# Optimization experiments

Measured on AMD Instinct MI355X. Metric: run time of the kernel, lower is better.

The kernel has to match this reference:

```python
import jax, jax.numpy as jnp
import numpy as np

QD, KD, HID, NH = 256, 320, 256, 8
NQ, NK, NB = 4096, 4096, 16
DH = HID // NH
EPS = 1e-5
SCALE = float(1.0 / np.sqrt(DH))


def setup_inputs() -> dict:
    key = jax.random.key(0)
    ks = jax.random.split(key, 12)
    s = 0.02
    return {
        "query_nodes": jax.random.normal(ks[0], (NQ, QD), jnp.float32),
        "key_nodes": jax.random.normal(ks[1], (NK, KD), jnp.float32),
        "Wq": jax.random.normal(ks[2], (QD, HID), jnp.float32) * s,
        "bq": jnp.zeros((HID,), jnp.float32),
        "Wk": jax.random.normal(ks[3], (KD, HID), jnp.float32) * s,
        "bk": jnp.zeros((HID,), jnp.float32),
        "Wv": jax.random.normal(ks[4], (KD, HID), jnp.float32) * s,
        "bv": jnp.zeros((HID,), jnp.float32),
        "in_proj_w": jax.random.normal(ks[5], (3 * HID, HID), jnp.float32) * s,
        "in_proj_b": jnp.zeros((3 * HID,), jnp.float32),
        "mha_ow": jax.random.normal(ks[6], (HID, HID), jnp.float32) * s,
        "mha_ob": jnp.zeros((HID,), jnp.float32),
        "Wo": jax.random.normal(ks[7], (HID, QD), jnp.float32) * s,
        "bo": jnp.zeros((QD,), jnp.float32),
        "ln_g": jnp.ones((QD,), jnp.float32),
        "ln_b": jnp.zeros((QD,), jnp.float32),
        "query_batch_idx": jnp.sort(jax.random.randint(ks[8], (NQ,), 0, NB, jnp.int32)),
        "key_batch_idx": jnp.sort(jax.random.randint(ks[9], (NK,), 0, NB, jnp.int32)),
    }


def reference(query_nodes, key_nodes, Wq, bq, Wk, bk, Wv, bv, in_proj_w, in_proj_b,
              mha_ow, mha_ob, Wo, bo, ln_g, ln_b, query_batch_idx, key_batch_idx):
    # outer projections
    q = query_nodes @ Wq + bq          # [NQ, HID]
    k = key_nodes @ Wk + bk            # [NK, HID]
    v = key_nodes @ Wv + bv            # [NK, HID]
    # nn.MultiheadAttention internal in_proj (weights stored [3H, H], applied as x @ W.T)
    q2 = q @ in_proj_w[:HID].T + in_proj_b[:HID]
    k2 = k @ in_proj_w[HID:2 * HID].T + in_proj_b[HID:2 * HID]
    v2 = v @ in_proj_w[2 * HID:].T + in_proj_b[2 * HID:]
    qh = q2.reshape(NQ, NH, DH)
    kh = k2.reshape(NK, NH, DH)
    vh = v2.reshape(NK, NH, DH)
    scores = jnp.einsum('qhd,khd->hqk', qh, kh) * SCALE   # [NH, NQ, NK]
    mask = query_batch_idx[:, None] != key_batch_idx[None, :]  # True = disallowed
    scores = jnp.where(mask[None], -jnp.inf, scores)
    attn = jax.nn.softmax(scores, axis=-1)
    ctx = jnp.einsum('hqk,khd->qhd', attn, vh).reshape(NQ, HID)
    ctx = ctx @ mha_ow + mha_ob        # MHA internal out_proj
    out = ctx @ Wo + bo                # module out_proj back to query_dim
    x = query_nodes + out              # residual (dropout is identity in eval)
    mu = jnp.mean(x, axis=-1, keepdims=True)
    var = jnp.mean((x - mu) ** 2, axis=-1, keepdims=True)
    return (x - mu) / jnp.sqrt(var + EPS) * ln_g + ln_b
```

## Files before the change

kernel.cpp:

```cpp
#include <hip/hip_runtime.h>
#include <hip/hip_bf16.h>
#include <math.h>

#define NQ 4096
#define NK 4096
#define QD 256
#define KD 320
#define HID 256
#define NH 8
#define DH 32
#define NB 16
#define LN_EPS 1e-5f
#define ATT_SCALE 0.17677669529663687f

typedef unsigned short ushort_t;
typedef __attribute__((ext_vector_type(8))) short bf16x8_t;
typedef __attribute__((ext_vector_type(4))) short bf16x4_t;
typedef __attribute__((ext_vector_type(4))) float f32x4_t;

#define OFF_Q2B   0
#define OFF_K2B   524288
#define OFF_V2B   1048576
#define OFF_CTXB  1572864
#define OFF_WQT   2097152
#define OFF_WKT   2129920
#define OFF_WVT   2170880
#define OFF_WOT   2211840
#define OFF_BEFF  2244608
#define OFF_KST   2245632
#define OFF_KEN   2245648
#define OFF_FLAG  2245664

struct KArgs {
    const void* in[18];
    float* ws;
    void* out;
};

__device__ __forceinline__ float bf16_bits_to_f(ushort_t s) {
    unsigned int u = (unsigned int)s << 16;
    float f;
    __builtin_memcpy(&f, &u, 4);
    return f;
}

__device__ __forceinline__ ushort_t f_to_bf16_bits(float v) {
    __hip_bfloat16 t = (__hip_bfloat16)v;
    ushort_t b;
    __builtin_memcpy(&b, &t, 2);
    return b;
}

template <bool F32>
__device__ __forceinline__ bf16x8_t ld8(const void* p, size_t idx) {
    if constexpr (!F32) {
        return *(const bf16x8_t*)((const ushort_t*)p + idx);
    } else {
        f32x4_t f0 = *(const f32x4_t*)((const float*)p + idx);
        f32x4_t f1 = *(const f32x4_t*)((const float*)p + idx + 4);
        bf16x8_t h;
#pragma unroll
        for (int e = 0; e < 4; ++e) h[e] = (short)f_to_bf16_bits(f0[e]);
#pragma unroll
        for (int e = 0; e < 4; ++e) h[4 + e] = (short)f_to_bf16_bits(f1[e]);
        return h;
    }
}

template <bool F32>
__device__ __forceinline__ float ld1f(const void* p, size_t idx) {
    if constexpr (F32) return ((const float*)p)[idx];
    else               return bf16_bits_to_f(((const ushort_t*)p)[idx]);
}

template <bool F32>
__device__ __forceinline__ ushort_t ld1h(const void* p, size_t idx) {
    if constexpr (F32) return f_to_bf16_bits(((const float*)p)[idx]);
    else               return ((const ushort_t*)p)[idx];
}

__device__ __forceinline__ int detect_flag(const void* probe_v, int tid) {
    __shared__ float s_red[4];
    const ushort_t* probe = (const ushort_t*)probe_v;
    float mx = 0.f;
    for (int i = tid; i < 4096; i += 256) {
        float f = fabsf(bf16_bits_to_f(probe[i]));
        if (!(f == f)) f = 1e38f;
        mx = fmaxf(mx, f);
    }
    for (int off = 32; off; off >>= 1) mx = fmaxf(mx, __shfl_xor(mx, off, 64));
    if ((tid & 63) == 0) s_red[tid >> 6] = mx;
    __syncthreads();
    float m2 = fmaxf(fmaxf(s_red[0], s_red[1]), fmaxf(s_red[2], s_red[3]));
    __syncthreads();
    return (m2 < 100.f) ? 1 : 0;
}

template <bool F32>
__device__ __forceinline__ void fuse_qkv_tile(const void* A, size_t abase,
                                              const void* B, ushort_t* Out,
                                              int N, int m0, int n0,
                                              int col, int quad) {
    f32x4_t acc[4];
#pragma unroll
    for (int t = 0; t < 4; ++t) acc[t] = (f32x4_t){0.f, 0.f, 0.f, 0.f};
    size_t aoff = abase + (size_t)(m0 + col) * 256 + quad * 8;
    size_t boff = (size_t)(n0 + col) * 256 + quad * 8;
#pragma unroll
    for (int kc = 0; kc < 256; kc += 32) {
        bf16x8_t af = ld8<F32>(A, aoff + kc);
#pragma unroll
        for (int t = 0; t < 4; ++t) {
            bf16x8_t bf = ld8<F32>(B, boff + (size_t)t * 16 * 256 + kc);
            acc[t] = __builtin_amdgcn_mfma_f32_16x16x32_bf16(af, bf, acc[t], 0, 0, 0);
        }
    }
#pragma unroll
    for (int t = 0; t < 4; ++t)
#pragma unroll
        for (int rr = 0; rr < 4; ++rr)
            Out[(size_t)(m0 + quad * 4 + rr) * N + n0 + t * 16 + col] =
                f_to_bf16_bits(acc[t][rr]);
}

template <bool F32>
__device__ __forceinline__ void fuse_o_tile(const void* Wo, const void* Mow,
                                            ushort_t* Out, int m0, int n0,
                                            int col, int quad) {
    f32x4_t acc[4];
#pragma unroll
    for (int t = 0; t < 4; ++t) acc[t] = (f32x4_t){0.f, 0.f, 0.f, 0.f};
#pragma unroll
    for (int kc = 0; kc < 256; kc += 32) {
        bf16x8_t af;
#pragma unroll
        for (int t = 0; t < 8; ++t)
            af[t] = (short)ld1h<F32>(Wo, (size_t)(kc + quad * 8 + t) * 256 + m0 + col);
#pragma unroll
        for (int t = 0; t < 4; ++t) {
            bf16x8_t bf = ld8<F32>(Mow, (size_t)(n0 + t * 16 + col) * 256 + quad * 8 + kc);
            acc[t] = __builtin_amdgcn_mfma_f32_16x16x32_bf16(af, bf, acc[t], 0, 0, 0);
        }
    }
#pragma unroll
    for (int t = 0; t < 4; ++t)
#pragma unroll
        for (int rr = 0; rr < 4; ++rr)
            Out[(size_t)(m0 + quad * 4 + rr) * 256 + n0 + t * 16 + col] =
                f_to_bf16_bits(acc[t][rr]);
}

template <bool F32>
__device__ __forceinline__ void bias_body(KArgs& a, float* ws, int m, int tid) {
    __shared__ float bsh[256];
    float* beff = ws + OFF_BEFF;
    if (m < 3) {
        const void* bsrc = (m == 0) ? a.in[3] : (m == 1) ? a.in[5] : a.in[7];
        bsh[tid] = ld1f<F32>(bsrc, tid);
        __syncthreads();
        float acc = 0.f;
        size_t row = (size_t)(m * 256 + tid) * 256;
#pragma unroll 4
        for (int kc = 0; kc < 256; kc += 8) {
            bf16x8_t wr = ld8<F32>(a.in[8], row + kc);
#pragma unroll
            for (int t = 0; t < 8; ++t)
                acc += bsh[kc + t] * bf16_bits_to_f((ushort_t)wr[t]);
        }
        acc += ld1f<F32>(a.in[9], m * 256 + tid);
        beff[m * 256 + tid] = acc;
    } else {
        bsh[tid] = ld1f<F32>(a.in[11], tid);
        __syncthreads();
        float acc = 0.f;
        for (int k = 0; k < 256; ++k)
            acc += bsh[k] * ld1f<F32>(a.in[12], (size_t)k * 256 + tid);
        acc += ld1f<F32>(a.in[13], tid);
        beff[3 * 256 + tid] = acc;
    }
}

__global__ __launch_bounds__(256) void k_fuse(KArgs a) {
    float* ws = a.ws;
    const int tid = threadIdx.x, bid = blockIdx.x;
    const int lane = tid & 63, wv = tid >> 6;
    const int col = lane & 15, quad = lane >> 4;
    int fl = detect_flag(a.in[0], tid);
    if (bid == 0 && tid == 0) *(int*)(ws + OFF_FLAG) = fl;

    if (bid < 16) {
        const int* kb = (const int*)a.in[17];
        int* kstart = (int*)(ws + OFF_KST);
        int* kend   = (int*)(ws + OFF_KEN);
        int j = bid * 256 + tid;
        if (j < NK) {
            int b = kb[j];
            if (j == 0) {
                for (int x = 0; x < b; ++x) { kstart[x] = 0; kend[x] = 0; }
                kstart[b] = 0;
            } else {
                int bp = kb[j - 1];
                if (bp != b) {
                    kend[bp] = j;
                    for (int x = bp + 1; x < b; ++x) { kstart[x] = j; kend[x] = j; }
                    kstart[b] = j;
                }
            }
            if (j == NK - 1) {
                kend[b] = NK;
                for (int x = b + 1; x < NB; ++x) { kstart[x] = NK; kend[x] = NK; }
            }
        }
    } else if (bid < 88) {
        int r = bid - 16;
        const void* A; const void* B; ushort_t* Out;
        size_t abase; int N, mb, nb, typ;
        if (r < 16)      { typ = 0; A = a.in[8]; abase = 0;      B = a.in[2]; Out = (ushort_t*)(ws + OFF_WQT); N = 256; mb = r >> 2; nb = r & 3; }
        else if (r < 36) { typ = 0; int rr = r - 16; A = a.in[8]; abase = 65536;  B = a.in[4]; Out = (ushort_t*)(ws + OFF_WKT); N = 320; mb = rr / 5; nb = rr % 5; }
        else if (r < 56) { typ = 0; int rr = r - 36; A = a.in[8]; abase = 131072; B = a.in[6]; Out = (ushort_t*)(ws + OFF_WVT); N = 320; mb = rr / 5; nb = rr % 5; }
        else             { typ = 1; int rr = r - 56; A = a.in[12]; abase = 0; B = a.in[10]; Out = (ushort_t*)(ws + OFF_WOT); N = 256; mb = rr >> 2; nb = rr & 3; }
        int m0 = mb * 64 + wv * 16, n0 = nb * 64;
        if (typ == 0) {
            if (fl) fuse_qkv_tile<false>(A, abase, B, Out, N, m0, n0, col, quad);
            else    fuse_qkv_tile<true >(A, abase, B, Out, N, m0, n0, col, quad);
        } else {
            if (fl) fuse_o_tile<false>(A, B, Out, m0, n0, col, quad);
            else    fuse_o_tile<true >(A, B, Out, m0, n0, col, quad);
        }
    } else {
        int m = bid - 88;
        if (fl) bias_body<false>(a, ws, m, tid);
        else    bias_body<true >(a, ws, m, tid);
    }
}

template <bool F32, int KK>
__device__ __forceinline__ void proj_body(const void* X, const ushort_t* WT,
                                          const float* bias, ushort_t* Z,
                                          int m0, int n0, int col, int quad) {
    f32x4_t acc[4];
#pragma unroll
    for (int t = 0; t < 4; ++t) acc[t] = (f32x4_t){0.f, 0.f, 0.f, 0.f};
    size_t aoff = (size_t)(m0 + col) * KK + quad * 8;
    const ushort_t* Wrow = WT + (size_t)(n0 + col) * KK + quad * 8;
#pragma unroll
    for (int kc = 0; kc < KK; kc += 32) {
        bf16x8_t af = ld8<F32>(X, aoff + kc);
#pragma unroll
        for (int t = 0; t < 4; ++t) {
            bf16x8_t bf = *(const bf16x8_t*)(Wrow + (size_t)t * 16 * KK + kc);
            acc[t] = __builtin_amdgcn_mfma_f32_16x16x32_bf16(af, bf, acc[t], 0, 0, 0);
        }
    }
#pragma unroll
    for (int t = 0; t < 4; ++t)
#pragma unroll
        for (int rr = 0; rr < 4; ++rr) {
            int n = n0 + t * 16 + col;
            Z[(size_t)(m0 + quad * 4 + rr) * 256 + n] =
                f_to_bf16_bits(acc[t][rr] + bias[n]);
        }
}

__global__ __launch_bounds__(256) void k_qkv(KArgs a) {
    float* ws = a.ws;
    const int tid = threadIdx.x, u = blockIdx.x;
    const int lane = tid & 63, wv = tid >> 6;
    const int col = lane & 15, quad = lane >> 4;
    const int fl = *(const int*)(ws + OFF_FLAG);
    const float* beff = ws + OFF_BEFF;

    if (u < 256) {
        int m0 = (u >> 2) * 64 + wv * 16, n0 = (u & 3) * 64;
        const ushort_t* WT = (const ushort_t*)(ws + OFF_WQT);
        ushort_t* Z = (ushort_t*)(ws + OFF_Q2B);
        if (fl) proj_body<false, 256>(a.in[0], WT, beff, Z, m0, n0, col, quad);
        else    proj_body<true , 256>(a.in[0], WT, beff, Z, m0, n0, col, quad);
    } else if (u < 512) {
        int uu = u - 256;
        int m0 = (uu >> 2) * 64 + wv * 16, n0 = (uu & 3) * 64;
        const ushort_t* WT = (const ushort_t*)(ws + OFF_WKT);
        ushort_t* Z = (ushort_t*)(ws + OFF_K2B);
        if (fl) proj_body<false, 320>(a.in[1], WT, beff + 256, Z, m0, n0, col, quad);
        else    proj_body<true , 320>(a.in[1], WT, beff + 256, Z, m0, n0, col, quad);
    } else {
        int uu = u - 512;
        int m0 = (uu >> 2) * 64 + wv * 16, n0 = (uu & 3) * 64;
        const ushort_t* WT = (const ushort_t*)(ws + OFF_WVT);
        ushort_t* Z = (ushort_t*)(ws + OFF_V2B);
        if (fl) proj_body<false, 320>(a.in[1], WT, beff + 512, Z, m0, n0, col, quad);
        else    proj_body<true , 320>(a.in[1], WT, beff + 512, Z, m0, n0, col, quad);
    }
}

#define CTXP 264

template <bool F32>
__device__ __forceinline__ void oln_part(KArgs& a, float* ws,
                                         const ushort_t ctxl[16][CTXP],
                                         float sred[8][16], float ssred[8][16],
                                         int q0, int wv, int col, int quad,
                                         int fl) {
    const ushort_t* wot  = (const ushort_t*)(ws + OFF_WOT);
    const float* beffO = ws + OFF_BEFF + 3 * 256;

    f32x4_t acc[2];
#pragma unroll
    for (int t = 0; t < 2; ++t) acc[t] = (f32x4_t){0.f, 0.f, 0.f, 0.f};
    const ushort_t* Wbase = wot + (size_t)col * 256 + quad * 8;
#pragma unroll
    for (int kc = 0; kc < 256; kc += 32) {
        bf16x8_t af = *(const bf16x8_t*)(&ctxl[col][quad * 8 + kc]);
#pragma unroll
        for (int tt = 0; tt < 2; ++tt) {
            int t = wv * 2 + tt;
            bf16x8_t bf = *(const bf16x8_t*)(Wbase + (size_t)t * 16 * 256 + kc);
            acc[tt] = __builtin_amdgcn_mfma_f32_16x16x32_bf16(af, bf, acc[tt], 0, 0, 0);
        }
    }
    float s_[4] = {0.f, 0.f, 0.f, 0.f};
    float ss_[4] = {0.f, 0.f, 0.f, 0.f};
#pragma unroll
    for (int tt = 0; tt < 2; ++tt) {
        int n = (wv * 2 + tt) * 16 + col;
        float b = beffO[n];
#pragma unroll
        for (int rr = 0; rr < 4; ++rr) {
            int m = q0 + quad * 4 + rr;
            float x = acc[tt][rr] + b + ld1f<F32>(a.in[0], (size_t)m * 256 + n);
            acc[tt][rr] = x;
            s_[rr] += x;
            ss_[rr] += x * x;
        }
    }
#pragma unroll
    for (int off = 1; off < 16; off <<= 1) {
#pragma unroll
        for (int rr = 0; rr < 4; ++rr) {
            s_[rr]  += __shfl_xor(s_[rr],  off, 16);
            ss_[rr] += __shfl_xor(ss_[rr], off, 16);
        }
    }
    if (col == 0) {
#pragma unroll
        for (int rr = 0; rr < 4; ++rr) {
            sred[wv][quad * 4 + rr]  = s_[rr];
            ssred[wv][quad * 4 + rr] = ss_[rr];
        }
    }
    __syncthreads();
    float mu[4], inv[4];
#pragma unroll
    for (int rr = 0; rr < 4; ++rr) {
        int row = quad * 4 + rr;
        float ts = 0.f, tss = 0.f;
#pragma unroll
        for (int w = 0; w < 8; ++w) { ts += sred[w][row]; tss += ssred[w][row]; }
        mu[rr] = ts * (1.f / QD);
        float var = tss * (1.f / QD) - mu[rr] * mu[rr];
        inv[rr] = rsqrtf(var + LN_EPS);
    }
#pragma unroll
    for (int tt = 0; tt < 2; ++tt) {
        int n = (wv * 2 + tt) * 16 + col;
        float g = ld1f<F32>(a.in[14], n), bb = ld1f<F32>(a.in[15], n);
#pragma unroll
        for (int rr = 0; rr < 4; ++rr) {
            int m = q0 + quad * 4 + rr;
            float y = (acc[tt][rr] - mu[rr]) * inv[rr] * g + bb;
            size_t idx = (size_t)m * 256 + n;
            if (fl) ((ushort_t*)a.out)[idx] = f_to_bf16_bits(y);
            else    ((float*)a.out)[idx] = y;
        }
    }
}

__global__ __launch_bounds__(512) void k_attn_oln(KArgs a) {
    __shared__ ushort_t ctxl[16][CTXP];
    __shared__ float sred[8][16], ssred[8][16];
    float* ws = a.ws;
    const ushort_t* q2b = (const ushort_t*)(ws + OFF_Q2B);
    const ushort_t* k2b = (const ushort_t*)(ws + OFF_K2B);
    const ushort_t* v2b = (const ushort_t*)(ws + OFF_V2B);
    const ushort_t* ctxb = (const ushort_t*)(ws + OFF_CTXB);
    const int* qb  = (const int*)a.in[16];
    const int* kst = (const int*)(ws + OFF_KST);
    const int* ken = (const int*)(ws + OFF_KEN);

    const int tid = threadIdx.x;
    const int lane = tid & 63, wv = tid >> 6;
    const int col = lane & 15, quad = lane >> 4;
    const int fl = *(const int*)(ws + OFF_FLAG);
    const int qt = blockIdx.x;
    const int q0 = qt * 16;
    const int h  = wv;

    {
        int m = tid >> 5, nblk = (tid & 31) * 8;
        *(bf16x8_t*)(&ctxl[m][nblk]) =
            *(const bf16x8_t*)(ctxb + (size_t)(q0 + m) * 256 + nblk);
    }
    __syncthreads();

    {
        int qq = q0 + col;
        int bq_ = qb[qq];
        int j0q = kst[bq_], j1q = ken[bq_];
        int jlo = j0q, jhi = j1q;
#pragma unroll
        for (int off = 1; off < 16; off <<= 1) {
            jlo = min(jlo, __shfl_xor(jlo, off, 64));
            jhi = max(jhi, __shfl_xor(jhi, off, 64));
        }

        bf16x8_t qf = *(const bf16x8_t*)(q2b + (size_t)qq * HID + h * DH + quad * 8);

        f32x4_t accO  = {0.f, 0.f, 0.f, 0.f};
        f32x4_t accO2 = {0.f, 0.f, 0.f, 0.f};
        float l_st = 0.f;

        for (int kt = jlo; kt < jhi; kt += 32) {
            int ktB = kt + 16;
            int krowA = kt + col;   if (krowA > NK - 1) krowA = NK - 1;
            int krowB = ktB + col;  if (krowB > NK - 1) krowB = NK - 1;
            bf16x8_t kfA = *(const bf16x8_t*)(k2b + (size_t)krowA * HID + h * DH + quad * 8);
            bf16x8_t kfB = *(const bf16x8_t*)(k2b + (size_t)krowB * HID + h * DH + quad * 8);
            ushort_t vrA[4], vrB[4];
#pragma unroll
            for (int j = 0; j < 4; ++j) {
                int vrowA = kt + quad * 4 + j;   if (vrowA > NK - 1) vrowA = NK - 1;
                int vrowB = ktB + quad * 4 + j;  if (vrowB > NK - 1) vrowB = NK - 1;
                vrA[j] = v2b[(size_t)vrowA * HID + h * DH + col];
                vrB[j] = v2b[(size_t)vrowB * HID + h * DH + col];
            }
            f32x4_t SA = __builtin_amdgcn_mfma_f32_16x16x32_bf16(
                kfA, qf, (f32x4_t){0.f, 0.f, 0.f, 0.f}, 0, 0, 0);
            f32x4_t SB = __builtin_amdgcn_mfma_f32_16x16x32_bf16(
                kfB, qf, (f32x4_t){0.f, 0.f, 0.f, 0.f}, 0, 0, 0);

            bf16x4_t pbA, vbA, pbB, vbB;
#pragma unroll
            for (int r = 0; r < 4; ++r) {
                int kkA = kt + quad * 4 + r;
                bool okA = (kkA >= j0q) && (kkA < j1q);
                float pA = okA ? __expf(SA[r] * ATT_SCALE) : 0.f;
                l_st += pA;
                pbA[r] = (short)f_to_bf16_bits(pA);
                vbA[r] = (short)vrA[r];
                int kkB = ktB + quad * 4 + r;
                bool okB = (kkB >= j0q) && (kkB < j1q);
                float pB = okB ? __expf(SB[r] * ATT_SCALE) : 0.f;
                l_st += pB;
                pbB[r] = (short)f_to_bf16_bits(pB);
                vbB[r] = (short)vrB[r];
            }
            accO  = __builtin_amdgcn_mfma_f32_16x16x16bf16_1k(pbA, vbA, accO,  0, 0, 0);
            accO2 = __builtin_amdgcn_mfma_f32_16x16x16bf16_1k(pbB, vbB, accO2, 0, 0, 0);
        }
#pragma unroll
        for (int r = 0; r < 4; ++r) accO[r] += accO2[r];

        l_st += __shfl_xor(l_st, 16, 64);
        l_st += __shfl_xor(l_st, 32, 64);

#pragma unroll
        for (int r = 0; r < 4; ++r) {
            int qrow_local = quad * 4 + r;
            float lq = __shfl(l_st, qrow_local, 64);
            float o = (lq > 0.f) ? accO[r] / lq : 0.f;
            ctxl[qrow_local][h * DH + col] = f_to_bf16_bits(o);
        }
    }
    __syncthreads();

    if (fl) oln_part<false>(a, ws, ctxl, sred, ssred, q0, wv, col, quad, fl);
    else    oln_part<true >(a, ws, ctxl, sred, ssred, q0, wv, col, quad, fl);
}

extern "C" void kernel_launch(void* const* d_in, const int* in_sizes, int n_in,
                              void* d_out, int out_size, void* d_ws, size_t ws_size,
                              hipStream_t stream) {
    KArgs a;
    for (int i = 0; i < 18; ++i) a.in[i] = d_in[i];
    a.ws = (float*)d_ws;
    a.out = d_out;

    k_fuse<<<92, 256, 0, stream>>>(a);
    k_qkv<<<768, 256, 0, stream>>>(a);
    k_attn_oln<<<256, 512, 0, stream>>>(a);
}
```

Before: 145.6 us.

## Stage QKV weight tiles in LDS and prefetch next K/V tile in attention loop

The QKV projection kernel now copies each block's 64-row weight slice into padded shared memory before the MFMA loop, so the four waves share one copy instead of each reading weights from global memory. The attention inner loop is software-pipelined: the K and V fragments for the next 32-key tile are loaded into a second register set while the current tile's MFMAs and exponentials run, hiding global load latency. The costs are extra LDS use and a barrier in the projection kernel, plus higher register pressure in the attention loop, which may lower occupancy.

```diff
diff --git a/kernel.cpp b/kernel.cpp
--- a/kernel.cpp
+++ b/kernel.cpp
@@ -234,21 +234,23 @@
     }
 }
 
+#define WPAD 8
+
 template <bool F32, int KK>
-__device__ __forceinline__ void proj_body(const void* X, const ushort_t* WT,
-                                          const float* bias, ushort_t* Z,
-                                          int m0, int n0, int col, int quad) {
+__device__ __forceinline__ void proj_body_lds(const void* X, const ushort_t* Wlds,
+                                              const float* bias, ushort_t* Z,
+                                              int m0, int n0, int col, int quad) {
     f32x4_t acc[4];
 #pragma unroll
     for (int t = 0; t < 4; ++t) acc[t] = (f32x4_t){0.f, 0.f, 0.f, 0.f};
     size_t aoff = (size_t)(m0 + col) * KK + quad * 8;
-    const ushort_t* Wrow = WT + (size_t)(n0 + col) * KK + quad * 8;
+    const ushort_t* Wrow = Wlds + (size_t)col * (KK + WPAD) + quad * 8;
 #pragma unroll
     for (int kc = 0; kc < KK; kc += 32) {
         bf16x8_t af = ld8<F32>(X, aoff + kc);
 #pragma unroll
         for (int t = 0; t < 4; ++t) {
-            bf16x8_t bf = *(const bf16x8_t*)(Wrow + (size_t)t * 16 * KK + kc);
+            bf16x8_t bf = *(const bf16x8_t*)(Wrow + (size_t)t * 16 * (KK + WPAD) + kc);
             acc[t] = __builtin_amdgcn_mfma_f32_16x16x32_bf16(af, bf, acc[t], 0, 0, 0);
         }
     }
@@ -262,7 +264,24 @@
         }
 }
 
+template <bool F32, int KK>
+__device__ __forceinline__ void qkv_seg(const void* X, const ushort_t* WT,
+                                        const float* bias, ushort_t* Z,
+                                        ushort_t* wlds, int uu,
+                                        int tid, int wv, int col, int quad) {
+    int m0 = (uu >> 2) * 64 + wv * 16, n0 = (uu & 3) * 64;
+    const int CH = KK / 8;
+    for (int c = tid; c < 64 * CH; c += 256) {
+        int r = c / CH, cc = c - r * CH;
+        *(bf16x8_t*)(wlds + (size_t)r * (KK + WPAD) + cc * 8) =
+            *(const bf16x8_t*)(WT + (size_t)(n0 + r) * KK + cc * 8);
+    }
+    __syncthreads();
+    proj_body_lds<F32, KK>(X, wlds, bias, Z, m0, n0, col, quad);
+}
+
 __global__ __launch_bounds__(256) void k_qkv(KArgs a) {
+    __shared__ ushort_t wlds[64 * (320 + WPAD)];
     float* ws = a.ws;
     const int tid = threadIdx.x, u = blockIdx.x;
     const int lane = tid & 63, wv = tid >> 6;
@@ -271,25 +290,22 @@
     const float* beff = ws + OFF_BEFF;
 
     if (u < 256) {
-        int m0 = (u >> 2) * 64 + wv * 16, n0 = (u & 3) * 64;
         const ushort_t* WT = (const ushort_t*)(ws + OFF_WQT);
         ushort_t* Z = (ushort_t*)(ws + OFF_Q2B);
-        if (fl) proj_body<false, 256>(a.in[0], WT, beff, Z, m0, n0, col, quad);
-        else    proj_body<true , 256>(a.in[0], WT, beff, Z, m0, n0, col, quad);
+        if (fl) qkv_seg<false, 256>(a.in[0], WT, beff, Z, wlds, u, tid, wv, col, quad);
+        else    qkv_seg<true , 256>(a.in[0], WT, beff, Z, wlds, u, tid, wv, col, quad);
     } else if (u < 512) {
         int uu = u - 256;
-        int m0 = (uu >> 2) * 64 + wv * 16, n0 = (uu & 3) * 64;
         const ushort_t* WT = (const ushort_t*)(ws + OFF_WKT);
         ushort_t* Z = (ushort_t*)(ws + OFF_K2B);
-        if (fl) proj_body<false, 320>(a.in[1], WT, beff + 256, Z, m0, n0, col, quad);
-        else    proj_body<true , 320>(a.in[1], WT, beff + 256, Z, m0, n0, col, quad);
+        if (fl) qkv_seg<false, 320>(a.in[1], WT, beff + 256, Z, wlds, uu, tid, wv, col, quad);
+        else    qkv_seg<true , 320>(a.in[1], WT, beff + 256, Z, wlds, uu, tid, wv, col, quad);
     } else {
         int uu = u - 512;
-        int m0 = (uu >> 2) * 64 + wv * 16, n0 = (uu & 3) * 64;
         const ushort_t* WT = (const ushort_t*)(ws + OFF_WVT);
         ushort_t* Z = (ushort_t*)(ws + OFF_V2B);
-        if (fl) proj_body<false, 320>(a.in[1], WT, beff + 512, Z, m0, n0, col, quad);
-        else    proj_body<true , 320>(a.in[1], WT, beff + 512, Z, m0, n0, col, quad);
+        if (fl) qkv_seg<false, 320>(a.in[1], WT, beff + 512, Z, wlds, uu, tid, wv, col, quad);
+        else    qkv_seg<true , 320>(a.in[1], WT, beff + 512, Z, wlds, uu, tid, wv, col, quad);
     }
 }
 
@@ -419,44 +435,65 @@
         f32x4_t accO2 = {0.f, 0.f, 0.f, 0.f};
         float l_st = 0.f;
 
-        for (int kt = jlo; kt < jhi; kt += 32) {
-            int ktB = kt + 16;
-            int krowA = kt + col;   if (krowA > NK - 1) krowA = NK - 1;
-            int krowB = ktB + col;  if (krowB > NK - 1) krowB = NK - 1;
-            bf16x8_t kfA = *(const bf16x8_t*)(k2b + (size_t)krowA * HID + h * DH + quad * 8);
-            bf16x8_t kfB = *(const bf16x8_t*)(k2b + (size_t)krowB * HID + h * DH + quad * 8);
-            ushort_t vrA[4], vrB[4];
-#pragma unroll
-            for (int j = 0; j < 4; ++j) {
-                int vrowA = kt + quad * 4 + j;   if (vrowA > NK - 1) vrowA = NK - 1;
-                int vrowB = ktB + quad * 4 + j;  if (vrowB > NK - 1) vrowB = NK - 1;
-                vrA[j] = v2b[(size_t)vrowA * HID + h * DH + col];
-                vrB[j] = v2b[(size_t)vrowB * HID + h * DH + col];
+#define ATT_LOAD(KT, KFA, KFB, VRA, VRB)                                          \
+        {                                                                         \
+            int ktB_ = (KT) + 16;                                                 \
+            int krA_ = (KT) + col;  if (krA_ > NK - 1) krA_ = NK - 1;             \
+            int krB_ = ktB_ + col;  if (krB_ > NK - 1) krB_ = NK - 1;             \
+            KFA = *(const bf16x8_t*)(k2b + (size_t)krA_ * HID + h * DH + quad * 8); \
+            KFB = *(const bf16x8_t*)(k2b + (size_t)krB_ * HID + h * DH + quad * 8); \
+            _Pragma("unroll")                                                     \
+            for (int j = 0; j < 4; ++j) {                                         \
+                int vrA_ = (KT) + quad * 4 + j;  if (vrA_ > NK - 1) vrA_ = NK - 1;  \
+                int vrB_ = ktB_ + quad * 4 + j;  if (vrB_ > NK - 1) vrB_ = NK - 1;  \
+                VRA[j] = v2b[(size_t)vrA_ * HID + h * DH + col];                  \
+                VRB[j] = v2b[(size_t)vrB_ * HID + h * DH + col];                  \
+            }                                                                     \
+        }
+
+        if (jlo < jhi) {
+            bf16x8_t kfA, kfB, kfA2, kfB2;
+            ushort_t vrA[4], vrB[4], vrA2[4], vrB2[4];
+            ATT_LOAD(jlo, kfA, kfB, vrA, vrB);
+            for (int kt = jlo; ; ) {
+                int ktn = kt + 32;
+                bool more = ktn < jhi;
+                if (more) ATT_LOAD(ktn, kfA2, kfB2, vrA2, vrB2);
+
+                int ktB = kt + 16;
+                f32x4_t SA = __builtin_amdgcn_mfma_f32_16x16x32_bf16(
+                    kfA, qf, (f32x4_t){0.f, 0.f, 0.f, 0.f}, 0, 0, 0);
+                f32x4_t SB = __builtin_amdgcn_mfma_f32_16x16x32_bf16(
+                    kfB, qf, (f32x4_t){0.f, 0.f, 0.f, 0.f}, 0, 0, 0);
+
+                bf16x4_t pbA, vbA, pbB, vbB;
+#pragma unroll
+                for (int r = 0; r < 4; ++r) {
+                    int kkA = kt + quad * 4 + r;
+                    bool okA = (kkA >= j0q) && (kkA < j1q);
+                    float pA = okA ? __expf(SA[r] * ATT_SCALE) : 0.f;
+                    l_st += pA;
+                    pbA[r] = (short)f_to_bf16_bits(pA);
+                    vbA[r] = (short)vrA[r];
+                    int kkB = ktB + quad * 4 + r;
+                    bool okB = (kkB >= j0q) && (kkB < j1q);
+                    float pB = okB ? __expf(SB[r] * ATT_SCALE) : 0.f;
+                    l_st += pB;
+                    pbB[r] = (short)f_to_bf16_bits(pB);
+                    vbB[r] = (short)vrB[r];
+                }
+                accO  = __builtin_amdgcn_mfma_f32_16x16x16bf16_1k(pbA, vbA, accO,  0, 0, 0);
+                accO2 = __builtin_amdgcn_mfma_f32_16x16x16bf16_1k(pbB, vbB, accO2, 0, 0, 0);
+
+                if (!more) break;
+                kfA = kfA2; kfB = kfB2;
+#pragma unroll
+                for (int j = 0; j < 4; ++j) { vrA[j] = vrA2[j]; vrB[j] = vrB2[j]; }
+                kt = ktn;
             }
-            f32x4_t SA = __builtin_amdgcn_mfma_f32_16x16x32_bf16(
-                kfA, qf, (f32x4_t){0.f, 0.f, 0.f, 0.f}, 0, 0, 0);
-            f32x4_t SB = __builtin_amdgcn_mfma_f32_16x16x32_bf16(
-                kfB, qf, (f32x4_t){0.f, 0.f, 0.f, 0.f}, 0, 0, 0);
-
-            bf16x4_t pbA, vbA, pbB, vbB;
-#pragma unroll
-            for (int r = 0; r < 4; ++r) {
-                int kkA = kt + quad * 4 + r;
-                bool okA = (kkA >= j0q) && (kkA < j1q);
-                float pA = okA ? __expf(SA[r] * ATT_SCALE) : 0.f;
-                l_st += pA;
-                pbA[r] = (short)f_to_bf16_bits(pA);
-                vbA[r] = (short)vrA[r];
-                int kkB = ktB + quad * 4 + r;
-                bool okB = (kkB >= j0q) && (kkB < j1q);
-                float pB = okB ? __expf(SB[r] * ATT_SCALE) : 0.f;
-                l_st += pB;
-                pbB[r] = (short)f_to_bf16_bits(pB);
-                vbB[r] = (short)vrB[r];
-            }
-            accO  = __builtin_amdgcn_mfma_f32_16x16x16bf16_1k(pbA, vbA, accO,  0, 0, 0);
-            accO2 = __builtin_amdgcn_mfma_f32_16x16x16bf16_1k(pbB, vbB, accO2, 0, 0, 0);
-        }
+        }
+#undef ATT_LOAD
+
 #pragma unroll
         for (int r = 0; r < 4; ++r) accO[r] += accO2[r];
 
```

Result: faster. 137.5 us (median of 2 runs) (-5.6%).
